# Kernel tuning notes

Measured on AMD Instinct MI355X. Metric: run time of the kernel, lower is better.

Reference implementation:

```python
import jax, jax.numpy as jnp
import numpy as np

B, IN, OUT, E, H, K = 8192, 1024, 256, 16, 512, 3
EPS = 1e-10


def setup_inputs() -> dict:
    key = jax.random.key(0)
    ks = jax.random.split(key, 5)
    scaled = lambda k, shape, fan: jax.random.normal(k, shape, jnp.float32) / np.sqrt(fan)
    return {
        "x": jax.random.normal(ks[0], (B, IN), jnp.float32),
        # torch init is zeros for w_gate (degenerate ties); use small random for a meaningful reference
        "w_gate": jax.random.normal(ks[1], (IN, E), jnp.float32) * 0.02,
        "W1": scaled(ks[2], (E, IN, H), IN),
        "b1": jnp.zeros((E, H), jnp.float32),
        "W2": scaled(ks[3], (E, H, OUT), H),
        "b2": jnp.zeros((E, OUT), jnp.float32),
    }


def _cv_squared(v):
    # torch .var() is unbiased (ddof=1)
    return jnp.var(v, ddof=1) / (jnp.mean(v) ** 2 + EPS)


def reference(x, w_gate, W1, b1, W2, b2):
    # --- top-k gating (eval mode: clean logits, no noise) ---
    logits = x @ w_gate                                   # [B, E]
    top_vals, top_idx = jax.lax.top_k(logits, K)          # [B, K]
    top_gates = jax.nn.softmax(top_vals, axis=-1)         # softmax over selected k
    rows = jnp.arange(logits.shape[0])[:, None]
    gates = jnp.zeros_like(logits).at[rows, top_idx].set(top_gates)  # sparse gates [B, E]

    # --- load-balancing loss ---
    importance = gates.sum(0)
    load = (gates > 0).sum(0).astype(jnp.float32)         # _gates_to_load (eval path)
    loss = _cv_squared(importance) + _cv_squared(load)

    # --- experts (MLP stand-in; dense compute, sparse combine via zero gates) ---
    h = jax.nn.relu(jnp.einsum('bi,eih->beh', x, W1) + b1)  # [B, E, H]
    expert_out = jnp.einsum('beh,eho->beo', h, W2) + b2     # [B, E, OUT]

    # combine: equivalent to SparseDispatcher gather/split/scatter-add with gate weighting
    y = jnp.einsum('be,beo->bo', gates, expert_out)         # [B, OUT]
    return y, loss
```

## Files before the change

kernel.cpp:

```cpp
#include <hip/hip_runtime.h>

#define B_ 8192
#define IN_ 1024
#define OUT_ 256
#define E_ 16
#define KTOP 3
#define H_ 512
#define MAXSLOTS 26624
#define NTILES 208
#define HBLK 16
#define GBLK 512

typedef __bf16 bf16;
typedef __bf16 bf16x4 __attribute__((ext_vector_type(4)));
typedef __bf16 bf16x8 __attribute__((ext_vector_type(8)));
typedef float f32x4 __attribute__((ext_vector_type(4)));

__device__ __forceinline__ void async16(const bf16* g, bf16* l) {
    __builtin_amdgcn_global_load_lds(
        (const __attribute__((address_space(1))) void*)g,
        (__attribute__((address_space(3))) void*)l,
        16, 0, 0);
}

__global__ __launch_bounds__(256) void k_stage1(
    const float* __restrict__ x, const float* __restrict__ wg,
    const float* __restrict__ W1, const float* __restrict__ W2,
    bf16* __restrict__ xbf, int* __restrict__ top_idx, float* __restrict__ top_gate,
    int* __restrict__ partial,
    bf16* __restrict__ w1t, bf16* __restrict__ w2t,
    int* __restrict__ row_ids, bf16* __restrict__ zero_row, int* __restrict__ tile_expert) {
    __shared__ __align__(16) float smem[16448];
    __shared__ int lcnt[16];
    int bx = blockIdx.x;
    int t = threadIdx.x;
    if (bx < GBLK) {
        float4* swgT4 = (float4*)smem;
        const float4* wg4 = (const float4*)wg;
        if (t < 16) lcnt[t] = 0;
#pragma unroll
        for (int i = 0; i < 16; i++) {
            int p = (t & 3) * 4 + ((t >> 2) & 3);
            int slot = i * 16 + (t >> 4);
            swgT4[p * 257 + slot] = wg4[i * 256 + t];
        }
        __syncthreads();
        int wv = t >> 6, lane = t & 63;
#pragma unroll
        for (int pr = 0; pr < 2; ++pr) {
            int row = bx * 16 + wv * 4 + pr * 2;
            const float4* xra = (const float4*)(x + (size_t)row * IN_);
            const float4* xrb = (const float4*)(x + (size_t)(row + 1) * IN_);
            float4 xa[4], xb4[4];
#pragma unroll
            for (int q = 0; q < 4; q++) { xa[q] = xra[lane + 64 * q]; xb4[q] = xrb[lane + 64 * q]; }
#pragma unroll
            for (int q = 0; q < 4; q++) {
                bf16x4 ca, cb;
                ca[0] = (bf16)xa[q].x; ca[1] = (bf16)xa[q].y; ca[2] = (bf16)xa[q].z; ca[3] = (bf16)xa[q].w;
                cb[0] = (bf16)xb4[q].x; cb[1] = (bf16)xb4[q].y; cb[2] = (bf16)xb4[q].z; cb[3] = (bf16)xb4[q].w;
                *(bf16x4*)(xbf + (size_t)row * IN_ + (size_t)(lane + 64 * q) * 4) = ca;
                *(bf16x4*)(xbf + (size_t)(row + 1) * IN_ + (size_t)(lane + 64 * q) * 4) = cb;
            }
            float acca[16], accb[16];
#pragma unroll
            for (int e = 0; e < 16; e++) { acca[e] = 0.f; accb[e] = 0.f; }
#pragma unroll
            for (int q = 0; q < 4; q++) {
                float sa[4] = {xa[q].x, xa[q].y, xa[q].z, xa[q].w};
                float sb[4] = {xb4[q].x, xb4[q].y, xb4[q].z, xb4[q].w};
#pragma unroll
                for (int jj = 0; jj < 4; jj++) {
#pragma unroll
                    for (int e4 = 0; e4 < 4; e4++) {
                        float4 w4 = swgT4[(e4 * 4 + jj) * 257 + lane + 64 * q];
                        acca[e4 * 4 + 0] += sa[jj] * w4.x;
                        acca[e4 * 4 + 1] += sa[jj] * w4.y;
                        acca[e4 * 4 + 2] += sa[jj] * w4.z;
                        acca[e4 * 4 + 3] += sa[jj] * w4.w;
                        accb[e4 * 4 + 0] += sb[jj] * w4.x;
                        accb[e4 * 4 + 1] += sb[jj] * w4.y;
                        accb[e4 * 4 + 2] += sb[jj] * w4.z;
                        accb[e4 * 4 + 3] += sb[jj] * w4.w;
                    }
                }
            }
#pragma unroll
            for (int e = 0; e < 16; e++) {
#pragma unroll
                for (int s = 32; s > 0; s >>= 1) {
                    acca[e] += __shfl_xor(acca[e], s, 64);
                    accb[e] += __shfl_xor(accb[e], s, 64);
                }
            }
            if (lane < 2) {
                float v[16];
#pragma unroll
                for (int e = 0; e < 16; e++) v[e] = lane ? accb[e] : acca[e];
                int rsel = row + lane;
                int idx[KTOP];
                float val[KTOP];
#pragma unroll
                for (int k = 0; k < KTOP; k++) {
                    int best = 0;
                    float bv = v[0];
                    for (int e = 1; e < 16; e++) {
                        if (v[e] > bv) { bv = v[e]; best = e; }
                    }
                    idx[k] = best; val[k] = bv; v[best] = -1e30f;
                }
                float e1 = __expf(val[1] - val[0]);
                float e2 = __expf(val[2] - val[0]);
                float inv = 1.f / (1.f + e1 + e2);
                float g[KTOP] = {inv, e1 * inv, e2 * inv};
#pragma unroll
                for (int k = 0; k < KTOP; k++) {
                    top_idx[rsel * KTOP + k] = idx[k];
                    top_gate[rsel * KTOP + k] = g[k];
                    atomicAdd(&lcnt[idx[k]], 1);
                }
            }
        }
        __syncthreads();
        if (t < 16) partial[bx * 16 + t] = lcnt[t];
        return;
    }
    if (bx >= 3072) {
        if (bx < 3176) {
            row_ids[(bx - 3072) * 256 + t] = -1;
        } else {
#pragma unroll
            for (int i = 0; i < 4; i++) zero_row[t * 4 + i] = (bf16)0.f;
            if (t < NTILES) tile_expert[t] = -1;
        }
        return;
    }
    float (*tile)[65] = (float(*)[65])smem;
    const float* in; bf16* out; int Kd, Nd, e, tk, tn;
    if (bx < 2560) {
        int b1x = bx - 512;
        in = W1; out = w1t; Kd = IN_; Nd = H_;
        e = b1x >> 7; int tt = b1x & 127; tk = tt >> 3; tn = tt & 7;
    } else {
        int b2x = bx - 2560;
        in = W2; out = w2t; Kd = H_; Nd = OUT_;
        e = b2x >> 5; int tt = b2x & 31; tk = tt >> 2; tn = tt & 3;
    }
    int r = t >> 6, c = t & 63;
    const float* src = in + ((size_t)e * Kd + tk * 64) * Nd + (size_t)tn * 64;
#pragma unroll
    for (int i = 0; i < 16; i++) {
        int rr = r + i * 4;
        tile[rr][c] = src[(size_t)rr * Nd + c];
    }
    __syncthreads();
    bf16* dst = out + ((size_t)e * Nd + tn * 64) * Kd + (size_t)tk * 64;
#pragma unroll
    for (int i = 0; i < 16; i++) {
        int rr = r + i * 4;
        dst[(size_t)rr * Kd + c] = (bf16)tile[c][rr];
    }
}

__global__ __launch_bounds__(256) void k_scatterscan(
    const int* __restrict__ top_idx, const float* __restrict__ top_gate,
    const int* __restrict__ partial,
    int* __restrict__ counts, int* __restrict__ tile_expert,
    int* __restrict__ row_ids, int* __restrict__ rowslot,
    float* __restrict__ partial_imp) {
    __shared__ int segsum[16][16];
    __shared__ int tote[16];
    __shared__ int sbase[16];
    __shared__ int lcnt[16];
    __shared__ float limp[16];
    int t = threadIdx.x;
    int blk = blockIdx.x;
    int e = t & 15, seg = t >> 4;
    int s = 0;
#pragma unroll
    for (int i = 0; i < GBLK / 16; i++) s += partial[(seg * (GBLK / 16) + i) * 16 + e];
    segsum[seg][e] = s;
    if (t < 16) { lcnt[t] = 0; limp[t] = 0.f; }
    __syncthreads();
    if (t < 16) {
        int total = 0, pre = 0;
        for (int sg = 0; sg < 16; sg++) {
            int v = segsum[sg][t];
            total += v;
            if (sg < blk) pre += v;
        }
        tote[t] = total;
        segsum[0][t] = pre;
    }
    __syncthreads();
    if (t < 16) {
        int off = 0;
        for (int ee = 0; ee < 16; ee++) {
            if (ee == t) break;
            off += (tote[ee] + 127) & ~127;
        }
        sbase[t] = off + segsum[0][t];
        if (blk == 0) {
            counts[t] = tote[t];
            int pd = (tote[t] + 127) & ~127;
            for (int tt = off >> 7; tt < (off + pd) >> 7; ++tt) tile_expert[tt] = t;
        }
    }
    __syncthreads();
#pragma unroll
    for (int j = 0; j < 6; j++) {
        int gid = blk * 1536 + j * 256 + t;
        int ee = top_idx[gid];
        float g = top_gate[gid];
        int rank = atomicAdd(&lcnt[ee], 1);
        atomicAdd(&limp[ee], g);
        int slot = sbase[ee] + rank;
        row_ids[slot] = gid / KTOP;
        rowslot[gid] = slot;
    }
    __syncthreads();
    if (t < 16) partial_imp[blk * 16 + t] = limp[t];
}

#define VWAIT(N) asm volatile("s_waitcnt vmcnt(" #N ")" ::: "memory")
__global__ __launch_bounds__(512) void k_fused(
    const bf16* __restrict__ xbf, const bf16* __restrict__ w1t,
    const float* __restrict__ b1, const bf16* __restrict__ w2t,
    const float* __restrict__ b2, const int* __restrict__ row_ids,
    const int* __restrict__ tile_expert, const bf16* __restrict__ zero_row,
    bf16* __restrict__ eout) {
    int bid = blockIdx.x;
    int tile = (bid & 7) * (NTILES / 8) + (bid >> 3);
    int e = tile_expert[tile];
    if (e < 0) return;
    int slot_base = tile * 128;
    __shared__ __align__(16) bf16 smem[69632];
    bf16* hs = smem;
    bf16* pb0 = smem + 32768;
    bf16* pb1 = smem + 32768 + 12288;
    bf16* pb2 = smem + 32768 + 24576;
    int t = threadIdx.x;
    int cg = (t & 3) ^ ((t >> 3) & 3);
    int rid = row_ids[slot_base + (t >> 2)];
    const bf16* gA = ((rid >= 0) ? xbf + (size_t)rid * IN_ : zero_row) + cg * 8;
    const bf16* gB1[2];
    const bf16* gB2[2];
#pragma unroll
    for (int j = 0; j < 2; j++) {
        int m = j * 128 + (t >> 2);
        gB1[j] = w1t + ((size_t)e * H_ + m) * IN_ + cg * 8;
        gB2[j] = w2t + ((size_t)e * OUT_ + m) * H_ + cg * 8;
    }
    int w = t >> 6, lane = t & 63;
    int wm = (w & 1) * 64, wn = (w >> 1) * 64;
    int lm = lane & 15, lq = lane >> 4;
    int aidx[4], bidx[4], hrow[4], hx[4];
#pragma unroll
    for (int i = 0; i < 4; i++) {
        int ra = wm + i * 16 + lm;
        int rb = wn + i * 16 + lm;
        aidx[i] = ra * 4 + (lq ^ ((ra >> 1) & 3));
        bidx[i] = rb * 4 + (lq ^ ((rb >> 1) & 3));
        hrow[i] = ra * 32;
        hx[i] = ra & 7;
    }
    float rbias1[2][4], rbias2[4];
#pragma unroll
    for (int c2 = 0; c2 < 2; ++c2)
#pragma unroll
        for (int ni = 0; ni < 4; ++ni) rbias1[c2][ni] = b1[e * H_ + c2 * 256 + wn + ni * 16 + lm];
#pragma unroll
    for (int ni = 0; ni < 4; ++ni) rbias2[ni] = b2[e * OUT_ + wn + ni * 16 + lm];
#pragma unroll
    for (int c2 = 0; c2 < 2; ++c2)
#pragma unroll
        for (int ni = 0; ni < 4; ++ni) asm volatile("" : "+v"(rbias1[c2][ni]));
#pragma unroll
    for (int ni = 0; ni < 4; ++ni) asm volatile("" : "+v"(rbias2[ni]));

    auto stageG1 = [&](bf16* buf, int c, int k) {
        async16(gA + k * 32, buf + t * 8);
        async16(gB1[0] + (size_t)c * (256 * IN_) + k * 32, buf + 4096 + t * 8);
        async16(gB1[1] + (size_t)c * (256 * IN_) + k * 32, buf + 4096 + (512 + t) * 8);
    };
    auto stageG2 = [&](bf16* buf, int c, int s) {
        const bf16* p0 = gB2[0] + c * 256 + s * 32;
        async16(p0, buf + t * 8);
        async16(gB2[1] + c * 256 + s * 32, buf + (512 + t) * 8);
        async16(p0, buf + t * 8);
    };

    f32x4 acc2[4][4] = {};
    bf16 *bufA = pb0, *bufB = pb1, *bufC = pb2;
    stageG1(bufA, 0, 0);
    stageG1(bufB, 0, 1);
#pragma unroll
    for (int c = 0; c < 2; ++c) {
        f32x4 acc1[4][4] = {};
        for (int k = 0; k < 32; ++k) {
            VWAIT(3);
            __builtin_amdgcn_s_barrier();
            __builtin_amdgcn_sched_barrier(0);
            const bf16x8* Av = (const bf16x8*)bufA;
            const bf16x8* Bv = (const bf16x8*)(bufA + 4096);
            bf16x8 af[4], bfv[4];
#pragma unroll
            for (int i = 0; i < 4; i++) af[i] = Av[aidx[i]];
#pragma unroll
            for (int i = 0; i < 4; i++) bfv[i] = Bv[bidx[i]];
#pragma unroll
            for (int mi = 0; mi < 4; mi++)
#pragma unroll
                for (int ni = 0; ni < 4; ni++)
                    acc1[mi][ni] = __builtin_amdgcn_mfma_f32_16x16x32_bf16(af[mi], bfv[ni], acc1[mi][ni], 0, 0, 0);
            if (k < 30) stageG1(bufC, c, k + 2);
            else        stageG2(bufC, c, k - 30);
            bf16* tmpb = bufA; bufA = bufB; bufB = bufC; bufC = tmpb;
        }
#pragma unroll
        for (int mi = 0; mi < 4; mi++) {
#pragma unroll
            for (int ni = 0; ni < 4; ni++) {
                int col = wn + ni * 16 + lm;
                float bias = rbias1[c][ni];
#pragma unroll
                for (int r = 0; r < 4; r++) {
                    int row = wm + mi * 16 + lq * 4 + r;
                    float v = acc1[mi][ni][r] + bias;
                    v = v > 0.f ? v : 0.f;
                    hs[row * 256 + (((col >> 3) ^ (row & 7)) << 3) + (col & 7)] = (bf16)v;
                }
            }
        }
        asm volatile("s_waitcnt lgkmcnt(0)" ::: "memory");
#pragma unroll
        for (int s = 0; s < 8; ++s) {
            if (c == 1 && s == 7) { VWAIT(0); } else { VWAIT(3); }
            __builtin_amdgcn_s_barrier();
            __builtin_amdgcn_sched_barrier(0);
            const bf16x8* Hv = (const bf16x8*)hs;
            const bf16x8* B2v = (const bf16x8*)bufA;
            bf16x8 af[4], bfv[4];
#pragma unroll
            for (int i = 0; i < 4; i++) af[i] = Hv[hrow[i] + ((s * 4 + lq) ^ hx[i])];
#pragma unroll
            for (int i = 0; i < 4; i++) bfv[i] = B2v[bidx[i]];
#pragma unroll
            for (int mi = 0; mi < 4; mi++)
#pragma unroll
                for (int ni = 0; ni < 4; ni++)
                    acc2[mi][ni] = __builtin_amdgcn_mfma_f32_16x16x32_bf16(af[mi], bfv[ni], acc2[mi][ni], 0, 0, 0);
            if (s < 6)       stageG2(bufC, c, s + 2);
            else if (c == 0) stageG1(bufC, 1, s - 6);
            bf16* tmpb = bufA; bufA = bufB; bufB = bufC; bufC = tmpb;
        }
    }
#pragma unroll
    for (int mi = 0; mi < 4; mi++) {
#pragma unroll
        for (int ni = 0; ni < 4; ni++) {
            int colg = wn + ni * 16 + lm;
            float bias = rbias2[ni];
#pragma unroll
            for (int r = 0; r < 4; r++) {
                int rowl = wm + mi * 16 + lq * 4 + r;
                eout[(size_t)(slot_base + rowl) * OUT_ + colg] = (bf16)(acc2[mi][ni][r] + bias);
            }
        }
    }
}

__global__ __launch_bounds__(256) void k_combine(
    const bf16* __restrict__ eout, const int* __restrict__ rowslot,
    const float* __restrict__ top_gate, float* __restrict__ y,
    const float* __restrict__ partial_imp, const int* __restrict__ counts,
    float* __restrict__ loss_out) {
    int t = threadIdx.x;
    if (blockIdx.x == B_ / 4) {
        __shared__ float imp[16];
        if (t < 16) {
            float s = 0.f;
#pragma unroll
            for (int b = 0; b < HBLK; b++) s += partial_imp[b * 16 + t];
            imp[t] = s;
        }
        __syncthreads();
        if (t == 0) {
            float si = 0.f, sl = 0.f;
            for (int e = 0; e < E_; e++) { si += imp[e]; sl += (float)counts[e]; }
            float mi_ = si / (float)E_, ml_ = sl / (float)E_;
            float vi = 0.f, vl = 0.f;
            for (int e = 0; e < E_; e++) {
                float d = imp[e] - mi_; vi += d * d;
                float d2 = (float)counts[e] - ml_; vl += d2 * d2;
            }
            vi /= (float)(E_ - 1); vl /= (float)(E_ - 1);
            *loss_out = vi / (mi_ * mi_ + 1e-10f) + vl / (ml_ * ml_ + 1e-10f);
        }
        return;
    }
    int b = blockIdx.x * 4 + (t >> 6);
    int lane = t & 63;
    int s0 = rowslot[b * 3], s1 = rowslot[b * 3 + 1], s2 = rowslot[b * 3 + 2];
    float g0 = top_gate[b * 3], g1 = top_gate[b * 3 + 1], g2 = top_gate[b * 3 + 2];
    bf16x4 v0 = *(const bf16x4*)(eout + (size_t)s0 * OUT_ + lane * 4);
    bf16x4 v1 = *(const bf16x4*)(eout + (size_t)s1 * OUT_ + lane * 4);
    bf16x4 v2 = *(const bf16x4*)(eout + (size_t)s2 * OUT_ + lane * 4);
    float4 r;
    r.x = g0 * (float)v0[0] + g1 * (float)v1[0] + g2 * (float)v2[0];
    r.y = g0 * (float)v0[1] + g1 * (float)v1[1] + g2 * (float)v2[1];
    r.z = g0 * (float)v0[2] + g1 * (float)v1[2] + g2 * (float)v2[2];
    r.w = g0 * (float)v0[3] + g1 * (float)v1[3] + g2 * (float)v2[3];
    ((float4*)y)[(size_t)b * 64 + lane] = r;
}

extern "C" void kernel_launch(void* const* d_in, const int* in_sizes, int n_in,
                              void* d_out, int out_size, void* d_ws, size_t ws_size,
                              hipStream_t stream) {
    (void)in_sizes; (void)n_in; (void)out_size; (void)ws_size;
    const float* x = (const float*)d_in[0];
    const float* wgate = (const float*)d_in[1];
    const float* W1 = (const float*)d_in[2];
    const float* b1 = (const float*)d_in[3];
    const float* W2 = (const float*)d_in[4];
    const float* b2 = (const float*)d_in[5];
    float* y = (float*)d_out;

    char* p = (char*)d_ws;
    auto alloc = [&](size_t bytes) {
        char* q = p;
        p += (bytes + 255) & ~(size_t)255;
        return q;
    };
    bf16* xbf = (bf16*)alloc((size_t)B_ * IN_ * 2);
    bf16* w1t = (bf16*)alloc((size_t)E_ * H_ * IN_ * 2);
    bf16* w2t = (bf16*)alloc((size_t)E_ * OUT_ * H_ * 2);
    bf16* eout = (bf16*)alloc((size_t)MAXSLOTS * OUT_ * 2);
    int* row_ids = (int*)alloc((size_t)MAXSLOTS * 4);
    int* rowslot = (int*)alloc((size_t)B_ * KTOP * 4);
    int* top_idx = (int*)alloc((size_t)B_ * KTOP * 4);
    float* top_gate = (float*)alloc((size_t)B_ * KTOP * 4);
    int* counts = (int*)alloc(E_ * 4);
    int* partial = (int*)alloc((size_t)GBLK * E_ * 4);
    float* partial_imp = (float*)alloc(HBLK * E_ * 4);
    int* tile_expert = (int*)alloc(NTILES * 4);
    bf16* zero_row = (bf16*)alloc(IN_ * 2);

    k_stage1<<<dim3(3177), dim3(256), 0, stream>>>(
        x, wgate, W1, W2, xbf, top_idx, top_gate, partial, w1t, w2t,
        row_ids, zero_row, tile_expert);
    k_scatterscan<<<dim3(HBLK), dim3(256), 0, stream>>>(
        top_idx, top_gate, partial, counts, tile_expert, row_ids, rowslot, partial_imp);
    k_fused<<<dim3(NTILES), dim3(512), 0, stream>>>(
        xbf, w1t, b1, w2t, b2, row_ids, tile_expert, zero_row, eout);
    k_combine<<<dim3(B_ / 4 + 1), dim3(256), 0, stream>>>(
        eout, rowslot, top_gate, y, partial_imp, counts, y + (size_t)B_ * OUT_);
}
```

Measured before the change: 180.3 us.

## Vectorize weight transpose, widen scatter-scan parallelism, raise MFMA wave priority

The weight transpose kernel now reads float4 rows and writes 8-wide bf16 vectors, where it previously used scalar loads and stores, cutting memory instruction count. The scatter-scan uses HBLK=32 blocks that each handle half as many assignments, summing 32 segments, to spread the atomic work over more blocks. The fused expert kernel wraps its MFMA bursts in s_setprio to favour waves doing matrix math over waves issuing loads. The HBLK change must match the launch geometry and the partial-count layout in the unseen host code.

```diff
diff --git a/kernel.cpp b/kernel.cpp
--- a/kernel.cpp
+++ b/kernel.cpp
@@ -8,7 +8,7 @@
 #define H_ 512
 #define MAXSLOTS 26624
 #define NTILES 208
-#define HBLK 16
+#define HBLK 32
 #define GBLK 512
 
 typedef __bf16 bf16;
@@ -146,19 +146,31 @@
         in = W2; out = w2t; Kd = H_; Nd = OUT_;
         e = b2x >> 5; int tt = b2x & 31; tk = tt >> 2; tn = tt & 3;
     }
-    int r = t >> 6, c = t & 63;
     const float* src = in + ((size_t)e * Kd + tk * 64) * Nd + (size_t)tn * 64;
-#pragma unroll
-    for (int i = 0; i < 16; i++) {
-        int rr = r + i * 4;
-        tile[rr][c] = src[(size_t)rr * Nd + c];
+    {
+        int c4 = (t & 15) * 4;
+#pragma unroll
+        for (int p = 0; p < 4; p++) {
+            int kr = p * 16 + (t >> 4);
+            float4 v = *(const float4*)(src + (size_t)kr * Nd + c4);
+            tile[kr][c4 + 0] = v.x;
+            tile[kr][c4 + 1] = v.y;
+            tile[kr][c4 + 2] = v.z;
+            tile[kr][c4 + 3] = v.w;
+        }
     }
     __syncthreads();
     bf16* dst = out + ((size_t)e * Nd + tn * 64) * Kd + (size_t)tk * 64;
-#pragma unroll
-    for (int i = 0; i < 16; i++) {
-        int rr = r + i * 4;
-        dst[(size_t)rr * Kd + c] = (bf16)tile[c][rr];
+    {
+        int k8 = (t & 7) * 8;
+#pragma unroll
+        for (int p = 0; p < 2; p++) {
+            int n = p * 32 + (t >> 3);
+            bf16x8 o;
+#pragma unroll
+            for (int j = 0; j < 8; j++) o[j] = (bf16)tile[k8 + j][n];
+            *(bf16x8*)(dst + (size_t)n * Kd + k8) = o;
+        }
     }
 }
 
@@ -168,23 +180,27 @@
     int* __restrict__ counts, int* __restrict__ tile_expert,
     int* __restrict__ row_ids, int* __restrict__ rowslot,
     float* __restrict__ partial_imp) {
-    __shared__ int segsum[16][16];
+    __shared__ int segsum[32][16];
     __shared__ int tote[16];
     __shared__ int sbase[16];
     __shared__ int lcnt[16];
     __shared__ float limp[16];
     int t = threadIdx.x;
     int blk = blockIdx.x;
-    int e = t & 15, seg = t >> 4;
-    int s = 0;
-#pragma unroll
-    for (int i = 0; i < GBLK / 16; i++) s += partial[(seg * (GBLK / 16) + i) * 16 + e];
-    segsum[seg][e] = s;
+    int e = t & 15, sg2 = t >> 4;
+#pragma unroll
+    for (int h = 0; h < 2; h++) {
+        int seg = sg2 + h * 16;
+        int s = 0;
+#pragma unroll
+        for (int i = 0; i < 16; i++) s += partial[(seg * 16 + i) * 16 + e];
+        segsum[seg][e] = s;
+    }
     if (t < 16) { lcnt[t] = 0; limp[t] = 0.f; }
     __syncthreads();
     if (t < 16) {
         int total = 0, pre = 0;
-        for (int sg = 0; sg < 16; sg++) {
+        for (int sg = 0; sg < 32; sg++) {
             int v = segsum[sg][t];
             total += v;
             if (sg < blk) pre += v;
@@ -208,8 +224,8 @@
     }
     __syncthreads();
 #pragma unroll
-    for (int j = 0; j < 6; j++) {
-        int gid = blk * 1536 + j * 256 + t;
+    for (int j = 0; j < 3; j++) {
+        int gid = blk * 768 + j * 256 + t;
         int ee = top_idx[gid];
         float g = top_gate[gid];
         int rank = atomicAdd(&lcnt[ee], 1);
@@ -308,11 +324,13 @@
             for (int i = 0; i < 4; i++) af[i] = Av[aidx[i]];
 #pragma unroll
             for (int i = 0; i < 4; i++) bfv[i] = Bv[bidx[i]];
+            __builtin_amdgcn_s_setprio(1);
 #pragma unroll
             for (int mi = 0; mi < 4; mi++)
 #pragma unroll
                 for (int ni = 0; ni < 4; ni++)
                     acc1[mi][ni] = __builtin_amdgcn_mfma_f32_16x16x32_bf16(af[mi], bfv[ni], acc1[mi][ni], 0, 0, 0);
+            __builtin_amdgcn_s_setprio(0);
             if (k < 30) stageG1(bufC, c, k + 2);
             else        stageG2(bufC, c, k - 30);
             bf16* tmpb = bufA; bufA = bufB; bufB = bufC; bufC = tmpb;
@@ -345,11 +363,13 @@
             for (int i = 0; i < 4; i++) af[i] = Hv[hrow[i] + ((s * 4 + lq) ^ hx[i])];
 #pragma unroll
             for (int i = 0; i < 4; i++) bfv[i] = B2v[bidx[i]];
+            __builtin_amdgcn_s_setprio(1);
 #pragma unroll
             for (int mi = 0; mi < 4; mi++)
 #pragma unroll
                 for (int ni = 0; ni < 4; ni++)
                     acc2[mi][ni] = __builtin_amdgcn_mfma_f32_16x16x32_bf16(af[mi], bfv[ni], acc2[mi][ni], 0, 0, 0);
+            __builtin_amdgcn_s_setprio(0);
             if (s < 6)       stageG2(bufC, c, s + 2);
             else if (c == 0) stageG1(bufC, 1, s - 6);
             bf16* tmpb = bufA; bufA = bufB; bufB = bufC; bufC = tmpb;
```

New measurement: 183.3 us. About the same (+1.7%).
